# Kernel optimization log

Hardware: AMD Instinct MI355X
Metric: run time of the kernel (lower is better)

## Reference

```python
import jax, jax.numpy as jnp
import numpy as np

N_NODES = 500000
N_EDGES = 8000000
LEN_SCALE = 20000.0


def setup_inputs() -> dict:
    key = jax.random.key(0)
    ks = jax.random.split(key, 10)
    inp = {
        'read_length': jax.random.randint(ks[0], (N_NODES,), 0, 20000, dtype=jnp.int64)
        if jax.config.read('jax_enable_x64') else jax.random.randint(ks[0], (N_NODES,), 0, 20000, dtype=jnp.int32),
        'edge_index': jax.random.randint(ks[1], (2, N_EDGES), 0, N_NODES, dtype=jnp.int32),
    }
    dims = [1, 4, 8, 16, 32]
    for i in range(4):
        fan_in, fan_out = dims[i], dims[i + 1]
        inp[f'W{i+1}'] = jax.random.normal(ks[2 + 2 * i], (fan_in, fan_out), jnp.float32) / np.sqrt(fan_in)
        inp[f'b{i+1}'] = jax.random.normal(ks[3 + 2 * i], (fan_out,), jnp.float32) * 0.01
    return inp


def _gcn_conv(x, W, b, src, dst, norm_e, dinv):
    # PyG GCNConv: linear first, then D^-1/2 (A+I) D^-1/2 aggregation, then bias.
    xw = x @ W                                              # [N, F_out]
    msg = xw[src] * norm_e[:, None]                         # [E, F_out]
    agg = jax.ops.segment_sum(msg, dst, num_segments=x.shape[0])
    # self-loop term handled analytically: norm for (i,i) is deg_i^-1
    return agg + xw * dinv[:, None] + b


def reference(read_length, edge_index, W1, b1, W2, b2, W3, b3, W4, b4):
    src, dst = edge_index[0], edge_index[1]
    # x = read_length / 20000, unsqueezed to [N, 1]
    x = (read_length.astype(jnp.float32) / LEN_SCALE)[:, None]
    N = x.shape[0]
    # degree with self-loops (edge weight 1)
    deg = jax.ops.segment_sum(jnp.ones_like(src, dtype=jnp.float32), dst, num_segments=N) + 1.0
    dinv_sqrt = jax.lax.rsqrt(deg)
    dinv = 1.0 / deg
    norm_e = dinv_sqrt[src] * dinv_sqrt[dst]                # [E]
    x = _gcn_conv(x, W1, b1, src, dst, norm_e, dinv)
    x = _gcn_conv(x, W2, b2, src, dst, norm_e, dinv)
    x = _gcn_conv(x, W3, b3, src, dst, norm_e, dinv)
    x = _gcn_conv(x, W4, b4, src, dst, norm_e, dinv)
    return x
```

## Files before the change

### kernel.cpp

```cpp
#include <hip/hip_runtime.h>
#include <hip/hip_bf16.h>


#define BLK  256
#define SBLK 1024
#define NB   512
#define BSH  10
#define PB   512
#define BUFCAP 15872
#define BUF2 18176
#define CAP  18432

__global__ void probe_i64(const int* __restrict__ rl32, int* __restrict__ flag,
                          int* __restrict__ cur) {
    __shared__ int sm[BLK];
    int t = threadIdx.x;
    if (blockIdx.x == 1) {
        for (int k = t; k < NB; k += BLK) cur[k] = 0;
        return;
    }
    int acc = 0;
    for (int k = t; k < 1024; k += blockDim.x)
        acc |= rl32[2 * k + 1];
    sm[t] = acc; __syncthreads();
    for (int off = BLK / 2; off > 0; off >>= 1) {
        if (t < off) sm[t] |= sm[t + off];
        __syncthreads();
    }
    if (t == 0) *flag = (sm[0] != 0) ? 1 : 0;
}

__global__ __launch_bounds__(SBLK)
void scatter(const int* __restrict__ src, const int* __restrict__ dst,
             int* __restrict__ cur, unsigned* __restrict__ epart, int E) {
    __shared__ unsigned buf[BUFCAP];
    __shared__ int h[NB];
    __shared__ int c0[NB];
    __shared__ int gpos[NB];
    int j = blockIdx.x, t = threadIdx.x;
    int chunk = (E + PB - 1) / PB;
    int beg = j * chunk, end = min(beg + chunk, E);
    for (int s = beg; s < end; s += BUFCAP) {
        int se = min(s + BUFCAP, end);
        for (int b = t; b < NB; b += SBLK) h[b] = 0;
        __syncthreads();
        for (int e = s + t; e < se; e += SBLK)
            atomicAdd(&h[((unsigned)dst[e]) >> BSH], 1);
        __syncthreads();
        if (t < NB) c0[t] = h[t];
        __syncthreads();
        for (int off = 1; off < NB; off <<= 1) {
            int add = 0;
            if (t < NB && t >= off) add = c0[t - off];
            __syncthreads();
            if (t < NB) c0[t] += add;
            __syncthreads();
        }
        if (t < NB) c0[t] -= h[t];
        __syncthreads();
        for (int e = s + t; e < se; e += SBLK) {
            unsigned d = (unsigned)dst[e];
            int b = d >> BSH;
            int slot = atomicAdd(&c0[b], 1);
            buf[slot] = ((d & 1023u) << 19) | (unsigned)src[e];
        }
        __syncthreads();
        if (t < NB) {
            int n = h[t];
            gpos[t] = (n > 0) ? atomicAdd(&cur[t], n) : 0;
        }
        __syncthreads();
        int w = t >> 6, lane = t & 63;
        for (int b = w; b < NB; b += (SBLK >> 6)) {
            int n = h[b];
            int lo = c0[b] - n;
            int gp = gpos[b];
            int left = CAP - gp;
            if (left < 0) left = 0;
            if (n > left) n = left;
            unsigned gb = (unsigned)b * CAP + (unsigned)gp;
            for (int k = lane; k < n; k += 64)
                epart[gb + k] = buf[lo + k];
        }
        __syncthreads();
    }
}

__global__ __launch_bounds__(1024)
void csr_build(const unsigned* __restrict__ epart, const int* __restrict__ cur,
               unsigned* __restrict__ epart2, int* __restrict__ rowp, int seg) {
    __shared__ unsigned buf[BUF2];
    __shared__ int sc[1024];
    __shared__ int cu[1024];
    __shared__ int s_beg, s_n;
    int b = blockIdx.x, t = threadIdx.x;
    if (t < 64) {
        int pre = 0, nn = 0;
        for (int k = t; k < NB; k += 64) {
            int v = min(cur[k], CAP);
            if (k < b) pre += v;
            if (k == b) nn = v;
        }
        for (int off = 1; off < 64; off <<= 1) {
            pre += __shfl_xor(pre, off);
            nn  += __shfl_xor(nn, off);
        }
        if (t == 0) { s_beg = pre; s_n = nn; }
    }
    sc[t] = 0;
    __syncthreads();
    int n = s_n;
    int gseg = b * CAP;
    int beg = seg ? gseg : s_beg;
    for (int e = t; e < n; e += 1024)
        atomicAdd(&sc[epart[gseg + e] >> 19], 1);
    __syncthreads();
    int v = sc[t];
    for (int off = 1; off < 1024; off <<= 1) {
        int add = (t >= off) ? sc[t - off] : 0;
        __syncthreads(); sc[t] += add; __syncthreads();
    }
    int start = sc[t] - v;
    rowp[b * 1025 + t] = beg + start;
    if (t == 1023) rowp[b * 1025 + 1024] = beg + n;
    cu[t] = start;
    __syncthreads();
    if (n <= BUF2) {
        for (int e = t; e < n; e += 1024) {
            unsigned p = epart[gseg + e];
            int slot = atomicAdd(&cu[p >> 19], 1);
            buf[slot] = p & 0x7FFFFu;
        }
        __syncthreads();
        for (int k = t; k < n; k += 1024)
            epart2[beg + k] = buf[k];
    } else if (!seg) {
        for (int e = t; e < n; e += 1024) {
            unsigned p = epart[gseg + e];
            int slot = atomicAdd(&cu[p >> 19], 1);
            epart2[beg + slot] = p & 0x7FFFFu;
        }
    }
}

__global__ void init_nodes(const int* __restrict__ rl, const int* __restrict__ rowp,
                           float* __restrict__ dinv, float2* __restrict__ v0,
                           const int* __restrict__ flag, int N,
                           const float* __restrict__ W1, const float* __restrict__ b1,
                           const float* __restrict__ W2, const float* __restrict__ b2,
                           const float* __restrict__ W3, const float* __restrict__ b3,
                           const float* __restrict__ W4, const float* __restrict__ b4,
                           float* __restrict__ c) {
    __shared__ float p3[16], q3[16], r3[16];
    int t = threadIdx.x;
    if (blockIdx.x == gridDim.x - 1) {
        if (t == 0) {
            float p2[8], q2[8];
            for (int j = 0; j < 8; ++j) {
                float s1 = 0.f, s2 = 0.f;
                for (int k = 0; k < 4; ++k) {
                    float w = W2[k * 8 + j];
                    s1 += W1[k] * w;
                    s2 += b1[k] * w;
                }
                p2[j] = s1; q2[j] = s2;
            }
            for (int m = 0; m < 16; ++m) {
                float s1 = 0.f, s2 = 0.f, s3 = 0.f;
                for (int j = 0; j < 8; ++j) {
                    float w = W3[j * 16 + m];
                    s1 += p2[j] * w; s2 += q2[j] * w;
                    s3 += b2[j] * w;
                }
                p3[m] = s1; q3[m] = s2; r3[m] = s3;
            }
        }
        __syncthreads();
        if (t < 32) {
            float c4 = 0.f, c3 = 0.f, c2 = 0.f, c1 = 0.f;
            for (int k = 0; k < 16; ++k) {
                float w = W4[k * 32 + t];
                c4 += p3[k] * w; c3 += q3[k] * w; c2 += r3[k] * w;
                c1 += b3[k] * w;
            }
            c[t] = c4; c[32 + t] = c3; c[64 + t] = c2; c[96 + t] = c1;
        }
        return;
    }
    int i = blockIdx.x * blockDim.x + t;
    if (i < N) {
        int v = (*flag) ? rl[i] : rl[2 * i];
        int rb = (i >> 10) * 1025 + (i & 1023);
        float d = (float)(rowp[rb + 1] - rowp[rb]) + 1.0f;
        dinv[i] = 1.0f / d;
        float rs = rsqrtf(d);
        float2 u; u.x = rs * ((float)v * (1.0f / 20000.0f)); u.y = rs;
        v0[i] = u;
    }
}

__global__ void gather_csr(const unsigned* __restrict__ epart2, const int* __restrict__ rowp,
                           const float2* __restrict__ vin, float2* __restrict__ vout,
                           const float* __restrict__ dinv, float* __restrict__ zsave, int N) {
    int t = blockIdx.x * blockDim.x + threadIdx.x;
    int i = t >> 3, l = t & 7;
    if (i >= N) return;
    int rb = (i >> 10) * 1025 + (i & 1023);
    int beg = rowp[rb], end = rowp[rb + 1];
    float a = 0.f, b = 0.f;
    int j = beg + l;
    for (; j + 8 < end; j += 16) {
        int s0 = epart2[j];
        int s1 = epart2[j + 8];
        float2 u0 = vin[s0];
        float2 u1 = vin[s1];
        a += u0.x + u1.x; b += u0.y + u1.y;
    }
    if (j < end) {
        float2 u = vin[epart2[j]];
        a += u.x; b += u.y;
    }
    a += __shfl_xor(a, 1); b += __shfl_xor(b, 1);
    a += __shfl_xor(a, 2); b += __shfl_xor(b, 2);
    a += __shfl_xor(a, 4); b += __shfl_xor(b, 4);
    if (l == 0) {
        float2 self = vin[i];
        float di = dinv[i];
        float2 o; o.x = (a + self.x) * di; o.y = (b + self.y) * di;
        vout[i] = o;
        if (zsave) zsave[i] = o.y;
    }
}

__global__ void gather_out(const unsigned* __restrict__ epart2, const int* __restrict__ rowp,
                           const float2* __restrict__ vin, const float* __restrict__ dinv,
                           const float* __restrict__ z1, const float* __restrict__ z2,
                           const float* __restrict__ z3, const float* __restrict__ c,
                           const float* __restrict__ b4, float* __restrict__ out, int N) {
    int t = blockIdx.x * blockDim.x + threadIdx.x;
    int i = t >> 3, l = t & 7;
    if (i >= N) return;
    int rb = (i >> 10) * 1025 + (i & 1023);
    int beg = rowp[rb], end = rowp[rb + 1];
    float a = 0.f;
    int j = beg + l;
    for (; j + 8 < end; j += 16) {
        int s0 = epart2[j];
        int s1 = epart2[j + 8];
        a += vin[s0].x + vin[s1].x;
    }
    if (j < end) a += vin[epart2[j]].x;
    a += __shfl_xor(a, 1);
    a += __shfl_xor(a, 2);
    a += __shfl_xor(a, 4);
    float di = dinv[i];
    float ox = (a + vin[i].x) * di;
    float sq = rsqrtf(di);
    float zz1 = z1[i], zz2 = z2[i], zz3 = z3[i];
    float4 cc4 = *(const float4*)&c[l * 4];
    float4 cc3 = *(const float4*)&c[32 + l * 4];
    float4 cc2 = *(const float4*)&c[64 + l * 4];
    float4 cc1 = *(const float4*)&c[96 + l * 4];
    float4 bb  = *(const float4*)&b4[l * 4];
    float4 o4;
    o4.x = sq * (ox * cc4.x + zz3 * cc3.x + zz2 * cc2.x + zz1 * cc1.x) + bb.x;
    o4.y = sq * (ox * cc4.y + zz3 * cc3.y + zz2 * cc2.y + zz1 * cc1.y) + bb.y;
    o4.z = sq * (ox * cc4.z + zz3 * cc3.z + zz2 * cc2.z + zz1 * cc1.z) + bb.z;
    o4.w = sq * (ox * cc4.w + zz3 * cc3.w + zz2 * cc2.w + zz1 * cc1.w) + bb.w;
    *(float4*)&out[(size_t)i * 32 + l * 4] = o4;
}

__global__ void write_out(const float2* __restrict__ v0, const float* __restrict__ z1,
                          const float* __restrict__ z2, const float* __restrict__ z3,
                          const float* __restrict__ dinv, const float* __restrict__ c,
                          const float* __restrict__ b4,
                          float* __restrict__ out, int N) {
    int t = blockIdx.x * blockDim.x + threadIdx.x;
    int i = t >> 5, f = t & 31;
    if (i < N) {
        float sq = rsqrtf(dinv[i]);
        float v = sq * (v0[i].x * c[f] + z3[i] * c[32 + f] + z2[i] * c[64 + f]
                        + z1[i] * c[96 + f])
                  + b4[f];
        out[(size_t)i * 32 + f] = v;
    }
}

extern "C" void kernel_launch(void* const* d_in, const int* in_sizes, int n_in,
                              void* d_out, int out_size, void* d_ws, size_t ws_size,
                              hipStream_t stream) {
    const int N = in_sizes[0];
    const int E = in_sizes[1] / 2;
    const int* rl  = (const int*)d_in[0];
    const int* src = (const int*)d_in[1];
    const int* dst = src + E;
    const float* W1 = (const float*)d_in[2];
    const float* b1 = (const float*)d_in[3];
    const float* W2 = (const float*)d_in[4];
    const float* b2 = (const float*)d_in[5];
    const float* W3 = (const float*)d_in[6];
    const float* b3 = (const float*)d_in[7];
    const float* W4 = (const float*)d_in[8];
    const float* b4 = (const float*)d_in[9];

    const int gbNode = (N + 1023) / 1024;

    char* w = (char*)d_ws;
    float2* v0   = (float2*)w;                w += (size_t)N * 8;
    float2* v1   = (float2*)w;                w += (size_t)N * 8;
    float*  dinv = (float*)w;                 w += (size_t)N * 4;
    float*  z1   = (float*)w;                 w += (size_t)N * 4;
    float*  z2   = (float*)w;                 w += (size_t)N * 4;
    float*  z3   = (float*)w;                 w += (size_t)N * 4;
    int*    rowp = (int*)w;                   w += (size_t)(gbNode * 1025 + 1) * 4;
    int*    cur  = (int*)w;                   w += NB * 4;
    float*  c    = (float*)w;                 w += 128 * 4;
    int*    flag = (int*)w;                   w += 16;
    size_t used = (size_t)(w - (char*)d_ws);
    used = (used + 255) & ~(size_t)255;
    bool fits = (used + (size_t)E * 4) <= ws_size;
    unsigned* epart  = (unsigned*)d_out;
    unsigned* epart2 = fits ? (unsigned*)((char*)d_ws + used) : epart;

    probe_i64<<<2, BLK, 0, stream>>>(rl, flag, cur);

    scatter<<<PB, SBLK, 0, stream>>>(src, dst, cur, epart, E);

    csr_build<<<gbNode, 1024, 0, stream>>>(epart, cur, epart2, rowp, fits ? 0 : 1);

    const int nInit = (N + BLK - 1) / BLK;
    init_nodes<<<nInit + 1, BLK, 0, stream>>>(rl, rowp, dinv, v0, flag, N,
                                              W1, b1, W2, b2, W3, b3, W4, b4, c);

    const int gbG = (8 * N + BLK - 1) / BLK;
    gather_csr<<<gbG, BLK, 0, stream>>>(epart2, rowp, v0, v1, dinv, z1, N);
    gather_csr<<<gbG, BLK, 0, stream>>>(epart2, rowp, v1, v0, dinv, z2, N);
    gather_csr<<<gbG, BLK, 0, stream>>>(epart2, rowp, v0, v1, dinv, z3, N);
    if (fits) {
        gather_out<<<gbG, BLK, 0, stream>>>(epart2, rowp, v1, dinv, z1, z2, z3,
                                            c, b4, (float*)d_out, N);
    } else {
        gather_csr<<<gbG, BLK, 0, stream>>>(epart2, rowp, v1, v0, dinv, (float*)nullptr, N);
        write_out<<<(N * 32 + BLK - 1) / BLK, BLK, 0, stream>>>(
            v0, z1, z2, z3, dinv, c, b4, (float*)d_out, N);
    }
}
```

Before: 403.2 us.

## Replace per-row CSR gathers with segmented edge-parallel reduction into shared memory

The row-pointer CSR is dropped. Edges stay dst-sorted within each 1024-node block with the local dst key packed in the high bits, and each gather becomes a block-wide edge-parallel pass. A wavefront segmented scan combines runs of equal keys before shared-memory atomics. Node initialisation (degree, dinv, v0) and the constant-folding work are fused into the CSR-building kernel, which removes one launch and the rowp round trip. The aim is to remove load imbalance and the eight-lanes-per-node waste on low-degree rows, at the cost of shuffle-scan work and shared atomics on every edge chunk.

Result: faster. 385.4 us (-4.4%).

```diff
diff --git a/kernel.cpp b/kernel.cpp
--- a/kernel.cpp
+++ b/kernel.cpp
@@ -87,73 +87,22 @@
 }
 
 __global__ __launch_bounds__(1024)
-void csr_build(const unsigned* __restrict__ epart, const int* __restrict__ cur,
-               unsigned* __restrict__ epart2, int* __restrict__ rowp, int seg) {
+void csr_init(const unsigned* __restrict__ epart, const int* __restrict__ cur,
+              const int* __restrict__ rl, const int* __restrict__ flag,
+              unsigned* __restrict__ epart2, int* __restrict__ bstart,
+              float* __restrict__ dinv, float2* __restrict__ v0, int N,
+              const float* __restrict__ W1, const float* __restrict__ b1,
+              const float* __restrict__ W2, const float* __restrict__ b2,
+              const float* __restrict__ W3, const float* __restrict__ b3,
+              const float* __restrict__ W4, const float* __restrict__ b4,
+              float* __restrict__ c, int seg) {
     __shared__ unsigned buf[BUF2];
     __shared__ int sc[1024];
     __shared__ int cu[1024];
     __shared__ int s_beg, s_n;
     int b = blockIdx.x, t = threadIdx.x;
-    if (t < 64) {
-        int pre = 0, nn = 0;
-        for (int k = t; k < NB; k += 64) {
-            int v = min(cur[k], CAP);
-            if (k < b) pre += v;
-            if (k == b) nn = v;
-        }
-        for (int off = 1; off < 64; off <<= 1) {
-            pre += __shfl_xor(pre, off);
-            nn  += __shfl_xor(nn, off);
-        }
-        if (t == 0) { s_beg = pre; s_n = nn; }
-    }
-    sc[t] = 0;
-    __syncthreads();
-    int n = s_n;
-    int gseg = b * CAP;
-    int beg = seg ? gseg : s_beg;
-    for (int e = t; e < n; e += 1024)
-        atomicAdd(&sc[epart[gseg + e] >> 19], 1);
-    __syncthreads();
-    int v = sc[t];
-    for (int off = 1; off < 1024; off <<= 1) {
-        int add = (t >= off) ? sc[t - off] : 0;
-        __syncthreads(); sc[t] += add; __syncthreads();
-    }
-    int start = sc[t] - v;
-    rowp[b * 1025 + t] = beg + start;
-    if (t == 1023) rowp[b * 1025 + 1024] = beg + n;
-    cu[t] = start;
-    __syncthreads();
-    if (n <= BUF2) {
-        for (int e = t; e < n; e += 1024) {
-            unsigned p = epart[gseg + e];
-            int slot = atomicAdd(&cu[p >> 19], 1);
-            buf[slot] = p & 0x7FFFFu;
-        }
-        __syncthreads();
-        for (int k = t; k < n; k += 1024)
-            epart2[beg + k] = buf[k];
-    } else if (!seg) {
-        for (int e = t; e < n; e += 1024) {
-            unsigned p = epart[gseg + e];
-            int slot = atomicAdd(&cu[p >> 19], 1);
-            epart2[beg + slot] = p & 0x7FFFFu;
-        }
-    }
-}
-
-__global__ void init_nodes(const int* __restrict__ rl, const int* __restrict__ rowp,
-                           float* __restrict__ dinv, float2* __restrict__ v0,
-                           const int* __restrict__ flag, int N,
-                           const float* __restrict__ W1, const float* __restrict__ b1,
-                           const float* __restrict__ W2, const float* __restrict__ b2,
-                           const float* __restrict__ W3, const float* __restrict__ b3,
-                           const float* __restrict__ W4, const float* __restrict__ b4,
-                           float* __restrict__ c) {
-    __shared__ float p3[16], q3[16], r3[16];
-    int t = threadIdx.x;
-    if (blockIdx.x == gridDim.x - 1) {
+    if (b == gridDim.x - 1) {
+        __shared__ float p3[16], q3[16], r3[16];
         if (t == 0) {
             float p2[8], q2[8];
             for (int j = 0; j < 8; ++j) {
@@ -187,87 +136,166 @@
         }
         return;
     }
-    int i = blockIdx.x * blockDim.x + t;
-    if (i < N) {
-        int v = (*flag) ? rl[i] : rl[2 * i];
-        int rb = (i >> 10) * 1025 + (i & 1023);
-        float d = (float)(rowp[rb + 1] - rowp[rb]) + 1.0f;
-        dinv[i] = 1.0f / d;
+    if (t < 64) {
+        int pre = 0, nn = 0;
+        for (int k = t; k < NB; k += 64) {
+            int v = min(cur[k], CAP);
+            if (k < b) pre += v;
+            if (k == b) nn = v;
+        }
+        for (int off = 1; off < 64; off <<= 1) {
+            pre += __shfl_xor(pre, off);
+            nn  += __shfl_xor(nn, off);
+        }
+        if (t == 0) { s_beg = pre; s_n = nn; }
+    }
+    sc[t] = 0;
+    __syncthreads();
+    int n = s_n;
+    int gseg = b * CAP;
+    int beg = seg ? gseg : s_beg;
+    if (t == 0) bstart[b] = beg;
+    if (b == gridDim.x - 2 && t == 1) bstart[b + 1] = beg + n;
+    for (int e = t; e < n; e += 1024)
+        atomicAdd(&sc[epart[gseg + e] >> 19], 1);
+    __syncthreads();
+    int v = sc[t];
+    for (int off = 1; off < 1024; off <<= 1) {
+        int add = (t >= off) ? sc[t - off] : 0;
+        __syncthreads(); sc[t] += add; __syncthreads();
+    }
+    cu[t] = sc[t] - v;
+    int gi = (b << 10) + t;
+    if (gi < N) {
+        int rv = (*flag) ? rl[gi] : rl[2 * gi];
+        float d = (float)v + 1.0f;
+        dinv[gi] = 1.0f / d;
         float rs = rsqrtf(d);
-        float2 u; u.x = rs * ((float)v * (1.0f / 20000.0f)); u.y = rs;
-        v0[i] = u;
-    }
-}
-
-__global__ void gather_csr(const unsigned* __restrict__ epart2, const int* __restrict__ rowp,
-                           const float2* __restrict__ vin, float2* __restrict__ vout,
-                           const float* __restrict__ dinv, float* __restrict__ zsave, int N) {
-    int t = blockIdx.x * blockDim.x + threadIdx.x;
-    int i = t >> 3, l = t & 7;
-    if (i >= N) return;
-    int rb = (i >> 10) * 1025 + (i & 1023);
-    int beg = rowp[rb], end = rowp[rb + 1];
-    float a = 0.f, b = 0.f;
-    int j = beg + l;
-    for (; j + 8 < end; j += 16) {
-        int s0 = epart2[j];
-        int s1 = epart2[j + 8];
-        float2 u0 = vin[s0];
-        float2 u1 = vin[s1];
-        a += u0.x + u1.x; b += u0.y + u1.y;
-    }
-    if (j < end) {
-        float2 u = vin[epart2[j]];
-        a += u.x; b += u.y;
-    }
-    a += __shfl_xor(a, 1); b += __shfl_xor(b, 1);
-    a += __shfl_xor(a, 2); b += __shfl_xor(b, 2);
-    a += __shfl_xor(a, 4); b += __shfl_xor(b, 4);
-    if (l == 0) {
-        float2 self = vin[i];
-        float di = dinv[i];
-        float2 o; o.x = (a + self.x) * di; o.y = (b + self.y) * di;
-        vout[i] = o;
-        if (zsave) zsave[i] = o.y;
-    }
-}
-
-__global__ void gather_out(const unsigned* __restrict__ epart2, const int* __restrict__ rowp,
-                           const float2* __restrict__ vin, const float* __restrict__ dinv,
-                           const float* __restrict__ z1, const float* __restrict__ z2,
-                           const float* __restrict__ z3, const float* __restrict__ c,
-                           const float* __restrict__ b4, float* __restrict__ out, int N) {
-    int t = blockIdx.x * blockDim.x + threadIdx.x;
-    int i = t >> 3, l = t & 7;
-    if (i >= N) return;
-    int rb = (i >> 10) * 1025 + (i & 1023);
-    int beg = rowp[rb], end = rowp[rb + 1];
-    float a = 0.f;
-    int j = beg + l;
-    for (; j + 8 < end; j += 16) {
-        int s0 = epart2[j];
-        int s1 = epart2[j + 8];
-        a += vin[s0].x + vin[s1].x;
-    }
-    if (j < end) a += vin[epart2[j]].x;
-    a += __shfl_xor(a, 1);
-    a += __shfl_xor(a, 2);
-    a += __shfl_xor(a, 4);
-    float di = dinv[i];
-    float ox = (a + vin[i].x) * di;
-    float sq = rsqrtf(di);
-    float zz1 = z1[i], zz2 = z2[i], zz3 = z3[i];
-    float4 cc4 = *(const float4*)&c[l * 4];
-    float4 cc3 = *(const float4*)&c[32 + l * 4];
-    float4 cc2 = *(const float4*)&c[64 + l * 4];
-    float4 cc1 = *(const float4*)&c[96 + l * 4];
-    float4 bb  = *(const float4*)&b4[l * 4];
-    float4 o4;
-    o4.x = sq * (ox * cc4.x + zz3 * cc3.x + zz2 * cc2.x + zz1 * cc1.x) + bb.x;
-    o4.y = sq * (ox * cc4.y + zz3 * cc3.y + zz2 * cc2.y + zz1 * cc1.y) + bb.y;
-    o4.z = sq * (ox * cc4.z + zz3 * cc3.z + zz2 * cc2.z + zz1 * cc1.z) + bb.z;
-    o4.w = sq * (ox * cc4.w + zz3 * cc3.w + zz2 * cc2.w + zz1 * cc1.w) + bb.w;
-    *(float4*)&out[(size_t)i * 32 + l * 4] = o4;
+        float2 u; u.x = rs * ((float)rv * (1.0f / 20000.0f)); u.y = rs;
+        v0[gi] = u;
+    }
+    __syncthreads();
+    if (n <= BUF2) {
+        for (int e = t; e < n; e += 1024) {
+            unsigned p = epart[gseg + e];
+            int slot = atomicAdd(&cu[p >> 19], 1);
+            buf[slot] = p;
+        }
+        __syncthreads();
+        for (int k = t; k < n; k += 1024)
+            epart2[beg + k] = buf[k];
+    } else if (!seg) {
+        for (int e = t; e < n; e += 1024) {
+            unsigned p = epart[gseg + e];
+            int slot = atomicAdd(&cu[p >> 19], 1);
+            epart2[beg + slot] = p;
+        }
+    }
+}
+
+__global__ __launch_bounds__(1024)
+void gather_seg(const unsigned* __restrict__ ep, const int* __restrict__ bstart,
+                const int* __restrict__ cur, int seg,
+                const float2* __restrict__ vin, float2* __restrict__ vout,
+                const float* __restrict__ dinv, float* __restrict__ zsave, int N) {
+    __shared__ float ax[1024];
+    __shared__ float ay[1024];
+    int b = blockIdx.x, t = threadIdx.x;
+    ax[t] = 0.f; ay[t] = 0.f;
+    __syncthreads();
+    int beg = bstart[b];
+    int n = seg ? min(cur[b], CAP) : (bstart[b + 1] - beg);
+    int end = beg + n;
+    int lane = t & 63;
+    for (int base = beg + (t - lane); base < end; base += 1024) {
+        int e = base + lane;
+        unsigned p = (e < end) ? ep[e] : 0xFFFFFFFFu;
+        int key = (int)(p >> 19);
+        float vx = 0.f, vy = 0.f;
+        if (e < end) {
+            float2 u = vin[p & 0x7FFFFu];
+            vx = u.x; vy = u.y;
+        }
+#pragma unroll
+        for (int off = 1; off < 64; off <<= 1) {
+            float ox = __shfl_up(vx, off);
+            float oy = __shfl_up(vy, off);
+            int ok = __shfl_up(key, off);
+            bool act = (lane >= off) && (ok == key);
+            vx += act ? ox : 0.f;
+            vy += act ? oy : 0.f;
+        }
+        int nk = __shfl_down(key, 1);
+        bool tail = (lane == 63) || (nk != key);
+        if (tail && key < 1024) {
+            atomicAdd(&ax[key], vx);
+            atomicAdd(&ay[key], vy);
+        }
+    }
+    __syncthreads();
+    int gi = (b << 10) + t;
+    if (gi < N) {
+        float2 self = vin[gi];
+        float di = dinv[gi];
+        float2 o; o.x = (ax[t] + self.x) * di; o.y = (ay[t] + self.y) * di;
+        vout[gi] = o;
+        if (zsave) zsave[gi] = o.y;
+    }
+}
+
+__global__ __launch_bounds__(1024)
+void gather_out_seg(const unsigned* __restrict__ ep, const int* __restrict__ bstart,
+                    const float2* __restrict__ vin, const float* __restrict__ dinv,
+                    const float* __restrict__ z1, const float* __restrict__ z2,
+                    const float* __restrict__ z3, const float* __restrict__ c,
+                    const float* __restrict__ b4, float* __restrict__ out, int N) {
+    __shared__ float ax[1024];
+    __shared__ float sqs[1024];
+    int b = blockIdx.x, t = threadIdx.x;
+    ax[t] = 0.f;
+    __syncthreads();
+    int beg = bstart[b], end = bstart[b + 1];
+    int lane = t & 63;
+    for (int base = beg + (t - lane); base < end; base += 1024) {
+        int e = base + lane;
+        unsigned p = (e < end) ? ep[e] : 0xFFFFFFFFu;
+        int key = (int)(p >> 19);
+        float vx = 0.f;
+        if (e < end) vx = vin[p & 0x7FFFFu].x;
+#pragma unroll
+        for (int off = 1; off < 64; off <<= 1) {
+            float ox = __shfl_up(vx, off);
+            int ok = __shfl_up(key, off);
+            bool act = (lane >= off) && (ok == key);
+            vx += act ? ox : 0.f;
+        }
+        int nk = __shfl_down(key, 1);
+        bool tail = (lane == 63) || (nk != key);
+        if (tail && key < 1024) atomicAdd(&ax[key], vx);
+    }
+    __syncthreads();
+    int gi = (b << 10) + t;
+    float ox = 0.f, sq = 0.f;
+    if (gi < N) {
+        float di = dinv[gi];
+        ox = (ax[t] + vin[gi].x) * di;
+        sq = rsqrtf(di);
+    }
+    __syncthreads();
+    ax[t] = ox; sqs[t] = sq;
+    __syncthreads();
+    int f = t & 31, half = t >> 5;
+    float c4 = c[f], c3 = c[32 + f], c2 = c[64 + f], c1 = c[96 + f], bb = b4[f];
+    int base_node = b << 10;
+    for (int p = 0; p < 32; ++p) {
+        int ln = p * 32 + half;
+        int g = base_node + ln;
+        if (g < N) {
+            float zz1 = z1[g], zz2 = z2[g], zz3 = z3[g];
+            float val = sqs[ln] * (ax[ln] * c4 + zz3 * c3 + zz2 * c2 + zz1 * c1) + bb;
+            out[(size_t)g * 32 + f] = val;
+        }
+    }
 }
 
 __global__ void write_out(const float2* __restrict__ v0, const float* __restrict__ z1,
@@ -312,7 +340,7 @@
     float*  z1   = (float*)w;                 w += (size_t)N * 4;
     float*  z2   = (float*)w;                 w += (size_t)N * 4;
     float*  z3   = (float*)w;                 w += (size_t)N * 4;
-    int*    rowp = (int*)w;                   w += (size_t)(gbNode * 1025 + 1) * 4;
+    int*    bstart = (int*)w;                 w += (NB + 1) * 4;
     int*    cur  = (int*)w;                   w += NB * 4;
     float*  c    = (float*)w;                 w += 128 * 4;
     int*    flag = (int*)w;                   w += 16;
@@ -321,26 +349,26 @@
     bool fits = (used + (size_t)E * 4) <= ws_size;
     unsigned* epart  = (unsigned*)d_out;
     unsigned* epart2 = fits ? (unsigned*)((char*)d_ws + used) : epart;
+    const int seg = fits ? 0 : 1;
 
     probe_i64<<<2, BLK, 0, stream>>>(rl, flag, cur);
 
     scatter<<<PB, SBLK, 0, stream>>>(src, dst, cur, epart, E);
 
-    csr_build<<<gbNode, 1024, 0, stream>>>(epart, cur, epart2, rowp, fits ? 0 : 1);
-
-    const int nInit = (N + BLK - 1) / BLK;
-    init_nodes<<<nInit + 1, BLK, 0, stream>>>(rl, rowp, dinv, v0, flag, N,
-                                              W1, b1, W2, b2, W3, b3, W4, b4, c);
-
-    const int gbG = (8 * N + BLK - 1) / BLK;
-    gather_csr<<<gbG, BLK, 0, stream>>>(epart2, rowp, v0, v1, dinv, z1, N);
-    gather_csr<<<gbG, BLK, 0, stream>>>(epart2, rowp, v1, v0, dinv, z2, N);
-    gather_csr<<<gbG, BLK, 0, stream>>>(epart2, rowp, v0, v1, dinv, z3, N);
+    csr_init<<<gbNode + 1, 1024, 0, stream>>>(epart, cur, rl, flag, epart2, bstart,
+                                              dinv, v0, N,
+                                              W1, b1, W2, b2, W3, b3, W4, b4, c, seg);
+
+    gather_seg<<<gbNode, 1024, 0, stream>>>(epart2, bstart, cur, seg, v0, v1, dinv, z1, N);
+    gather_seg<<<gbNode, 1024, 0, stream>>>(epart2, bstart, cur, seg, v1, v0, dinv, z2, N);
+    gather_seg<<<gbNode, 1024, 0, stream>>>(epart2, bstart, cur, seg, v0, v1, dinv, z3, N);
     if (fits) {
-        gather_out<<<gbG, BLK, 0, stream>>>(epart2, rowp, v1, dinv, z1, z2, z3,
-                                            c, b4, (float*)d_out, N);
+        gather_out_seg<<<gbNode, 1024, 0, stream>>>(epart2, bstart, v1, dinv,
+                                                    z1, z2, z3, c, b4,
+                                                    (float*)d_out, N);
     } else {
-        gather_csr<<<gbG, BLK, 0, stream>>>(epart2, rowp, v1, v0, dinv, (float*)nullptr, N);
+        gather_seg<<<gbNode, 1024, 0, stream>>>(epart2, bstart, cur, seg, v1, v0, dinv,
+                                                (float*)nullptr, N);
         write_out<<<(N * 32 + BLK - 1) / BLK, BLK, 0, stream>>>(
             v0, z1, z2, z3, dinv, c, b4, (float*)d_out, N);
     }
```
